# Kernel optimization log

Hardware: AMD Instinct MI355X
Metric: run time of the kernel (lower is better)

Reference implementation:

```python
import jax, jax.numpy as jnp
import numpy as np

N_NODES = 50000
NEG_SLOPE = 0.2  # PyG GATConv leaky_relu default


def _gat_layer(x, src, dst, W, a_src, a_dst, bias, heads, ch):
    n = x.shape[0]
    h = (x @ W).reshape(n, heads, ch)                    # [N,H,C]
    alpha_s = jnp.sum(h * a_src, axis=-1)                # [N,H]
    alpha_d = jnp.sum(h * a_dst, axis=-1)                # [N,H]
    e = alpha_s[src] + alpha_d[dst]                      # [E,H]
    e = jnp.where(e > 0, e, NEG_SLOPE * e)               # leaky_relu
    # segment softmax over incoming edges of each dst node
    m = jax.ops.segment_max(e, dst, num_segments=n)      # [N,H]
    m = jnp.where(jnp.isfinite(m), m, 0.0)
    ex = jnp.exp(e - m[dst])                             # [E,H]
    denom = jax.ops.segment_sum(ex, dst, num_segments=n) # [N,H]
    alpha = ex / (denom[dst] + 1e-16)                    # [E,H]
    msg = alpha[:, :, None] * h[src]                     # [E,H,C]
    out = jax.ops.segment_sum(msg, dst, num_segments=n)  # [N,H,C]
    return out.reshape(n, heads * ch) + bias


def setup_inputs() -> dict:
    key = jax.random.key(0)
    ks = jax.random.split(key, 10)
    F_in, H1, C1, C2 = 256, 8, 32, 32
    E = 500000
    x = jax.random.normal(ks[0], (N_NODES, F_in), dtype=jnp.float32)
    edge_index = jax.random.randint(ks[1], (2, E), 0, N_NODES, dtype=jnp.int64)
    s1 = 1.0 / np.sqrt(F_in)
    s2 = 1.0 / np.sqrt(H1 * C1)
    return {
        "x": x,
        "edge_index": edge_index,
        "W1": jax.random.normal(ks[2], (F_in, H1 * C1), dtype=jnp.float32) * s1,
        "a_src1": jax.random.normal(ks[3], (H1, C1), dtype=jnp.float32) * s2,
        "a_dst1": jax.random.normal(ks[4], (H1, C1), dtype=jnp.float32) * s2,
        "b1": jnp.zeros((H1 * C1,), dtype=jnp.float32),
        "W2": jax.random.normal(ks[5], (H1 * C1, C2), dtype=jnp.float32) * s2,
        "a_src2": jax.random.normal(ks[6], (1, C2), dtype=jnp.float32) * (1.0 / np.sqrt(C2)),
        "a_dst2": jax.random.normal(ks[7], (1, C2), dtype=jnp.float32) * (1.0 / np.sqrt(C2)),
        "b2": jnp.zeros((C2,), dtype=jnp.float32),
    }


def reference(x, edge_index, W1, a_src1, a_dst1, b1, W2, a_src2, a_dst2, b2):
    n = x.shape[0]
    # add self-loops (PyG GATConv default add_self_loops=True)
    loop = jnp.arange(n, dtype=edge_index.dtype)
    src = jnp.concatenate([edge_index[0], loop])
    dst = jnp.concatenate([edge_index[1], loop])
    h = _gat_layer(x, src, dst, W1, a_src1, a_dst1, b1, heads=8, ch=32)
    h = jax.nn.elu(h)
    h = _gat_layer(h, src, dst, W2, a_src2, a_dst2, b2, heads=1, ch=32)
    return jax.nn.log_softmax(h, axis=1)
```

## Files before the change

kernel.cpp:

```cpp
#include <hip/hip_runtime.h>
#include <math.h>


typedef __attribute__((ext_vector_type(8))) short bf16x8;
typedef __attribute__((ext_vector_type(4))) float f32x4;

__device__ __forceinline__ float bf2f(ushort u) {
    union { uint i; float f; } v; v.i = ((uint)u) << 16; return v.f;
}
__device__ __forceinline__ ushort f2bf(float f) {
    union { float f; uint i; } v; v.f = f;
    uint r = v.i + 0x7FFFu + ((v.i >> 16) & 1u);
    return (ushort)(r >> 16);
}
__device__ __forceinline__ uint pack2(float a, float b) {
    return (uint)f2bf(a) | ((uint)f2bf(b) << 16);
}

__global__ void detect_kernel(const int* ei32, int* flag) {
    __shared__ int cnt;
    if (threadIdx.x == 0) cnt = 0;
    __syncthreads();
    int nz = 0;
    for (int i = threadIdx.x; i < 1024; i += blockDim.x)
        if (ei32[2 * i + 1] != 0) nz++;
    atomicAdd(&cnt, nz);
    __syncthreads();
    if (threadIdx.x == 0) *flag = (cnt > 16) ? 1 : 0;
}

__global__ void decode_degree_kernel(const void* ei, int E, int ET, int N,
                                     const int* __restrict__ flag,
                                     int* __restrict__ src, int* __restrict__ dst,
                                     int* __restrict__ deg) {
    int k = blockIdx.x * blockDim.x + threadIdx.x;
    if (k >= ET) return;
    int s, d;
    if (k < E) {
        if (*flag) {
            const int* p = (const int*)ei;
            s = p[k]; d = p[E + k];
        } else {
            const long long* p = (const long long*)ei;
            s = (int)p[k]; d = (int)p[E + k];
        }
    } else {
        s = d = k - E;
    }
    s = min(max(s, 0), N - 1);
    d = min(max(d, 0), N - 1);
    src[k] = s; dst[k] = d;
    atomicAdd(&deg[d], 1);
}

__global__ __launch_bounds__(256) void scanA_kernel(const int* __restrict__ deg,
                                                    int* __restrict__ bsum, int n) {
    int i = blockIdx.x * 256 + threadIdx.x;
    int v = (i < n) ? deg[i] : 0;
#pragma unroll
    for (int s = 1; s < 64; s <<= 1) v += __shfl_xor(v, s, 64);
    __shared__ int ws[4];
    int lane = threadIdx.x & 63, wid = threadIdx.x >> 6;
    if (lane == 0) ws[wid] = v;
    __syncthreads();
    if (threadIdx.x == 0) bsum[blockIdx.x] = ws[0] + ws[1] + ws[2] + ws[3];
}

__global__ __launch_bounds__(1024) void scanB_kernel(int* __restrict__ bsum, int nb) {
    int t = threadIdx.x;
    int v = (t < nb) ? bsum[t] : 0;
    __shared__ int sm[1024];
    sm[t] = v;
    __syncthreads();
    for (int s = 1; s < 1024; s <<= 1) {
        int a = (t >= s) ? sm[t - s] : 0;
        __syncthreads();
        sm[t] += a;
        __syncthreads();
    }
    if (t < nb) bsum[t] = sm[t] - v;
}

__global__ __launch_bounds__(256) void scanC_kernel(const int* __restrict__ deg,
                                                    const int* __restrict__ bsum,
                                                    int* __restrict__ off, int n) {
    int t = threadIdx.x;
    int i = blockIdx.x * 256 + t;
    int v = (i < n) ? deg[i] : 0;
    int incl = v;
    int lane = t & 63, wid = t >> 6;
#pragma unroll
    for (int s = 1; s < 64; s <<= 1) {
        int a = __shfl_up(incl, s, 64);
        if (lane >= s) incl += a;
    }
    __shared__ int wsum[4];
    if (lane == 63) wsum[wid] = incl;
    __syncthreads();
    int wo = 0;
    for (int w = 0; w < wid; w++) wo += wsum[w];
    if (i < n) off[i + 1] = bsum[blockIdx.x] + wo + incl;
    if (i == 0) off[0] = 0;
}

__global__ void scatter_kernel(const int* __restrict__ src, const int* __restrict__ dst,
                               int ET, const int* __restrict__ off,
                               int* __restrict__ cursor, int* __restrict__ esrc) {
    int k = blockIdx.x * blockDim.x + threadIdx.x;
    if (k >= ET) return;
    int d = dst[k];
    int p = atomicAdd(&cursor[d], 1);
    esrc[off[d] + p] = src[k];
}

__global__ __launch_bounds__(256) void convert_w_kernel(
        const float* __restrict__ W1, const float* __restrict__ W2,
        ushort* __restrict__ w1t, ushort* __restrict__ w2t) {
    int bid = blockIdx.x;
    if (bid < 64) {
        __shared__ float tile[32][33];
        int tx = threadIdx.x & 31, ty = threadIdx.x >> 5;
        int bx = bid & 7, by = bid >> 3;
        for (int i = 0; i < 32; i += 8)
            tile[ty + i][tx] = W1[(by * 32 + ty + i) * 256 + bx * 32 + tx];
        __syncthreads();
        for (int i = 0; i < 32; i += 8)
            w1t[(bx * 32 + ty + i) * 256 + by * 32 + tx] = f2bf(tile[tx][ty + i]);
    } else {
        int idx = (bid - 64) * 256 + threadIdx.x;
        int c = idx >> 8, k = idx & 255;
        w2t[idx] = f2bf(W2[k * 32 + c]);
    }
}

#define LDA 72
__global__ __launch_bounds__(256) void gemm1_mfma(
        const float* __restrict__ x,
        const ushort* __restrict__ w1t,
        ushort* __restrict__ h1b,
        int N) {
    __shared__ ushort Al[128 * LDA];
    __shared__ ushort Bl[128 * LDA];
    int t = threadIdx.x;
    int row0 = blockIdx.x * 128;
    int n0 = blockIdx.y * 128;
    int lane = t & 63, wid = t >> 6;
    int wr = wid >> 1, wc = wid & 1;

    f32x4 acc[4][4] = {};

    int sr = t >> 1, scs = (t & 1) * 32;
    for (int k0 = 0; k0 < 256; k0 += 64) {
        {
            int gr = row0 + sr;
            float4 f[8];
            if (gr < N) {
                const float4* g = (const float4*)(x + (size_t)gr * 256 + k0 + scs);
#pragma unroll
                for (int q = 0; q < 8; q++) f[q] = g[q];
            } else {
#pragma unroll
                for (int q = 0; q < 8; q++) f[q] = float4{0.f, 0.f, 0.f, 0.f};
            }
            uint4* d = (uint4*)&Al[sr * LDA + scs];
#pragma unroll
            for (int p = 0; p < 4; p++) {
                uint4 u;
                u.x = pack2(f[2 * p].x, f[2 * p].y);
                u.y = pack2(f[2 * p].z, f[2 * p].w);
                u.z = pack2(f[2 * p + 1].x, f[2 * p + 1].y);
                u.w = pack2(f[2 * p + 1].z, f[2 * p + 1].w);
                d[p] = u;
            }
        }
        {
            const uint4* g = (const uint4*)(w1t + (size_t)(n0 + sr) * 256 + k0 + scs);
            uint4* d = (uint4*)&Bl[sr * LDA + scs];
            d[0] = g[0]; d[1] = g[1]; d[2] = g[2]; d[3] = g[3];
        }
        __syncthreads();

#pragma unroll
        for (int ks = 0; ks < 2; ks++) {
            int kk = ks * 32 + (lane >> 4) * 8;
            bf16x8 af[4], bfr[4];
#pragma unroll
            for (int mi = 0; mi < 4; mi++) {
                int r = wr * 64 + mi * 16 + (lane & 15);
                af[mi] = *(const bf16x8*)&Al[r * LDA + kk];
            }
#pragma unroll
            for (int ni = 0; ni < 4; ni++) {
                int r = wc * 64 + ni * 16 + (lane & 15);
                bfr[ni] = *(const bf16x8*)&Bl[r * LDA + kk];
            }
#pragma unroll
            for (int mi = 0; mi < 4; mi++)
#pragma unroll
                for (int ni = 0; ni < 4; ni++)
                    acc[mi][ni] = __builtin_amdgcn_mfma_f32_16x16x32_bf16(
                        af[mi], bfr[ni], acc[mi][ni], 0, 0, 0);
        }
        __syncthreads();
    }

#pragma unroll
    for (int mi = 0; mi < 4; mi++)
#pragma unroll
        for (int ni = 0; ni < 4; ni++) {
            int gc = n0 + wc * 64 + ni * 16 + (lane & 15);
#pragma unroll
            for (int j = 0; j < 4; j++) {
                int gr = row0 + wr * 64 + mi * 16 + (lane >> 4) * 4 + j;
                if (gr < N) h1b[(size_t)gr * 256 + gc] = f2bf(acc[mi][ni][j]);
            }
        }
}

__global__ __launch_bounds__(256) void alpha1_kernel(
        const ushort* __restrict__ h1b,
        const float* __restrict__ a_src1, const float* __restrict__ a_dst1,
        float* __restrict__ as1, float* __restrict__ ad1, int N) {
    int t = threadIdx.x;
    int g = t >> 5, l = t & 31;
    int node = blockIdx.x * 8 + g;
    if (node >= N) return;
    bf16x8 hv = *(const bf16x8*)&h1b[(size_t)node * 256 + l * 8];
    float s = 0.f, d = 0.f;
#pragma unroll
    for (int i = 0; i < 8; i++) {
        float h = bf2f((ushort)hv[i]);
        s = fmaf(h, a_src1[l * 8 + i], s);
        d = fmaf(h, a_dst1[l * 8 + i], d);
    }
    s += __shfl_xor(s, 1); s += __shfl_xor(s, 2);
    d += __shfl_xor(d, 1); d += __shfl_xor(d, 2);
    if ((l & 3) == 0) {
        as1[node * 8 + (l >> 2)] = s;
        ad1[node * 8 + (l >> 2)] = d;
    }
}

#define FMA8(W, V)                                                      \
    c0 = fmaf(W, bf2f((ushort)((V).x & 0xffffu)), c0);                  \
    c1 = fmaf(W, bf2f((ushort)((V).x >> 16)), c1);                      \
    c2 = fmaf(W, bf2f((ushort)((V).y & 0xffffu)), c2);                  \
    c3 = fmaf(W, bf2f((ushort)((V).y >> 16)), c3);                      \
    c4 = fmaf(W, bf2f((ushort)((V).z & 0xffffu)), c4);                  \
    c5 = fmaf(W, bf2f((ushort)((V).z >> 16)), c5);                      \
    c6 = fmaf(W, bf2f((ushort)((V).w & 0xffffu)), c6);                  \
    c7 = fmaf(W, bf2f((ushort)((V).w >> 16)), c7);

__global__ __launch_bounds__(256) void agg1f_kernel(
        const ushort* __restrict__ h1b,
        const float* __restrict__ as1, const float* __restrict__ ad1,
        const float* __restrict__ b1,
        const int* __restrict__ off, const int* __restrict__ esrc,
        ushort* __restrict__ hactb, int N) {
    __shared__ float s_w[8][32][8];
    int t = threadIdx.x;
    int slot = t >> 5;
    int node = blockIdx.x * 8 + slot;
    int l = t & 31;
    if (node >= N) return;
    int beg = off[node], end = off[node + 1];
    int deg = end - beg;
    int h = l & 7, q = l >> 3;
    float adv = ad1[node * 8 + h];
    int head2 = l >> 2;
    int ch0 = l * 8;
    const ushort* hb = h1b + ch0;
    float c0 = 0.f, c1 = 0.f, c2 = 0.f, c3 = 0.f;
    float c4 = 0.f, c5 = 0.f, c6 = 0.f, c7 = 0.f;

    if (deg <= 32) {
        float e_r[8];
#pragma unroll
        for (int r = 0; r < 8; r++) {
            int j = beg + r * 4 + q;
            float e = -3.0e38f;
            if (j < end) {
                e = as1[esrc[j] * 8 + h] + adv;
                e = (e > 0.f) ? e : 0.2f * e;
            }
            e_r[r] = e;
        }
        float m = e_r[0];
#pragma unroll
        for (int r = 1; r < 8; r++) m = fmaxf(m, e_r[r]);
        m = fmaxf(m, __shfl_xor(m, 8, 32));
        m = fmaxf(m, __shfl_xor(m, 16, 32));
        float dnm = 0.f;
#pragma unroll
        for (int r = 0; r < 8; r++)
            if (beg + r * 4 + q < end) dnm += __expf(e_r[r] - m);
        dnm += __shfl_xor(dnm, 8, 32);
        dnm += __shfl_xor(dnm, 16, 32);
        float inv = 1.f / (dnm + 1e-16f);
#pragma unroll
        for (int r = 0; r < 8; r++) {
            int j = beg + r * 4 + q;
            if (j < end) s_w[slot][r * 4 + q][h] = __expf(e_r[r] - m) * inv;
        }
        const float* wp = &s_w[slot][0][head2];
        int j = beg;
        for (; j + 4 <= end; j += 4) {
            int k = j - beg;
            int s0 = esrc[j + 0], s1 = esrc[j + 1], s2 = esrc[j + 2], s3 = esrc[j + 3];
            float w0 = wp[(k + 0) * 8];
            float w1 = wp[(k + 1) * 8];
            float w2 = wp[(k + 2) * 8];
            float w3 = wp[(k + 3) * 8];
            uint4 v0 = *(const uint4*)(hb + (size_t)s0 * 256);
            uint4 v1 = *(const uint4*)(hb + (size_t)s1 * 256);
            uint4 v2 = *(const uint4*)(hb + (size_t)s2 * 256);
            uint4 v3 = *(const uint4*)(hb + (size_t)s3 * 256);
            FMA8(w0, v0);
            FMA8(w1, v1);
            FMA8(w2, v2);
            FMA8(w3, v3);
        }
        for (; j < end; j++) {
            int s0 = esrc[j];
            float w = wp[(j - beg) * 8];
            uint4 v = *(const uint4*)(hb + (size_t)s0 * 256);
            FMA8(w, v);
        }
    } else {
        float m = -3.0e38f;
        for (int j0 = beg; j0 < end; j0 += 4) {
            int j = j0 + q;
            if (j < end) {
                float e = as1[esrc[j] * 8 + h] + adv;
                e = (e > 0.f) ? e : 0.2f * e;
                m = fmaxf(m, e);
            }
        }
        m = fmaxf(m, __shfl_xor(m, 8, 32));
        m = fmaxf(m, __shfl_xor(m, 16, 32));
        float dnm = 0.f;
        for (int j0 = beg; j0 < end; j0 += 4) {
            int j = j0 + q;
            if (j < end) {
                float e = as1[esrc[j] * 8 + h] + adv;
                e = (e > 0.f) ? e : 0.2f * e;
                dnm += __expf(e - m);
            }
        }
        dnm += __shfl_xor(dnm, 8, 32);
        dnm += __shfl_xor(dnm, 16, 32);
        float inv = 1.f / (dnm + 1e-16f);
        float m2   = __shfl(m, head2, 32);
        float inv2 = __shfl(inv, head2, 32);
        float adv2 = __shfl(adv, head2, 32);
        const float* asp = as1 + head2;
        for (int j = beg; j < end; j++) {
            int s0 = esrc[j];
            float e = asp[s0 * 8] + adv2;
            e = (e > 0.f) ? e : 0.2f * e;
            float w = __expf(e - m2) * inv2;
            uint4 v = *(const uint4*)(hb + (size_t)s0 * 256);
            FMA8(w, v);
        }
    }

    float4 bv0 = *(const float4*)&b1[ch0];
    float4 bv1 = *(const float4*)&b1[ch0 + 4];
    float o0 = c0 + bv0.x, o1 = c1 + bv0.y, o2 = c2 + bv0.z, o3 = c3 + bv0.w;
    float o4 = c4 + bv1.x, o5 = c5 + bv1.y, o6 = c6 + bv1.z, o7 = c7 + bv1.w;
    o0 = (o0 > 0.f) ? o0 : (__expf(o0) - 1.f);
    o1 = (o1 > 0.f) ? o1 : (__expf(o1) - 1.f);
    o2 = (o2 > 0.f) ? o2 : (__expf(o2) - 1.f);
    o3 = (o3 > 0.f) ? o3 : (__expf(o3) - 1.f);
    o4 = (o4 > 0.f) ? o4 : (__expf(o4) - 1.f);
    o5 = (o5 > 0.f) ? o5 : (__expf(o5) - 1.f);
    o6 = (o6 > 0.f) ? o6 : (__expf(o6) - 1.f);
    o7 = (o7 > 0.f) ? o7 : (__expf(o7) - 1.f);
    uint4 r;
    r.x = pack2(o0, o1);
    r.y = pack2(o2, o3);
    r.z = pack2(o4, o5);
    r.w = pack2(o6, o7);
    *(uint4*)(hactb + (size_t)node * 256 + ch0) = r;
}

__global__ __launch_bounds__(256) void gemm2_mfma(
        const ushort* __restrict__ hactb,
        const ushort* __restrict__ w2t,
        float* __restrict__ h2, int N) {
    __shared__ ushort Al[128 * LDA];
    __shared__ ushort Bl[32 * LDA];
    int t = threadIdx.x;
    int row0 = blockIdx.x * 128;
    int lane = t & 63, wid = t >> 6;

    f32x4 acc[2][2] = {};

    int sr = t >> 1, scs = (t & 1) * 32;
    for (int k0 = 0; k0 < 256; k0 += 64) {
        {
            int gr = row0 + sr;
            uint4 v0 = {0,0,0,0}, v1 = {0,0,0,0}, v2 = {0,0,0,0}, v3 = {0,0,0,0};
            if (gr < N) {
                const uint4* g = (const uint4*)(hactb + (size_t)gr * 256 + k0 + scs);
                v0 = g[0]; v1 = g[1]; v2 = g[2]; v3 = g[3];
            }
            uint4* d = (uint4*)&Al[sr * LDA + scs];
            d[0] = v0; d[1] = v1; d[2] = v2; d[3] = v3;
        }
        if (t < 64) {
            const uint4* g = (const uint4*)(w2t + (size_t)sr * 256 + k0 + scs);
            uint4* d = (uint4*)&Bl[sr * LDA + scs];
            d[0] = g[0]; d[1] = g[1]; d[2] = g[2]; d[3] = g[3];
        }
        __syncthreads();

#pragma unroll
        for (int ks = 0; ks < 2; ks++) {
            int kk = ks * 32 + (lane >> 4) * 8;
            bf16x8 af[2], bfr[2];
#pragma unroll
            for (int mi = 0; mi < 2; mi++) {
                int r = wid * 32 + mi * 16 + (lane & 15);
                af[mi] = *(const bf16x8*)&Al[r * LDA + kk];
            }
#pragma unroll
            for (int ni = 0; ni < 2; ni++) {
                int r = ni * 16 + (lane & 15);
                bfr[ni] = *(const bf16x8*)&Bl[r * LDA + kk];
            }
#pragma unroll
            for (int mi = 0; mi < 2; mi++)
#pragma unroll
                for (int ni = 0; ni < 2; ni++)
                    acc[mi][ni] = __builtin_amdgcn_mfma_f32_16x16x32_bf16(
                        af[mi], bfr[ni], acc[mi][ni], 0, 0, 0);
        }
        __syncthreads();
    }

#pragma unroll
    for (int mi = 0; mi < 2; mi++)
#pragma unroll
        for (int ni = 0; ni < 2; ni++) {
            int gc = ni * 16 + (lane & 15);
#pragma unroll
            for (int j = 0; j < 4; j++) {
                int gr = row0 + wid * 32 + mi * 16 + (lane >> 4) * 4 + j;
                if (gr < N) h2[(size_t)gr * 32 + gc] = acc[mi][ni][j];
            }
        }
}

__global__ __launch_bounds__(256) void alpha2_kernel(
        const float* __restrict__ h2,
        const float* __restrict__ a_src2, const float* __restrict__ a_dst2,
        float* __restrict__ as2, float* __restrict__ ad2, int N) {
    int t = threadIdx.x;
    int g = t >> 3, q = t & 7;
    int node = blockIdx.x * 32 + g;
    if (node >= N) return;
    float4 v = *(const float4*)&h2[(size_t)node * 32 + q * 4];
    float4 sa = *(const float4*)&a_src2[q * 4];
    float4 da = *(const float4*)&a_dst2[q * 4];
    float s = v.x * sa.x + v.y * sa.y + v.z * sa.z + v.w * sa.w;
    float d = v.x * da.x + v.y * da.y + v.z * da.z + v.w * da.w;
    s += __shfl_xor(s, 1, 8); s += __shfl_xor(s, 2, 8); s += __shfl_xor(s, 4, 8);
    d += __shfl_xor(d, 1, 8); d += __shfl_xor(d, 2, 8); d += __shfl_xor(d, 4, 8);
    if (q == 0) { as2[node] = s; ad2[node] = d; }
}

__global__ __launch_bounds__(256) void agg2f_kernel(
        const float* __restrict__ h2,
        const float* __restrict__ as2, const float* __restrict__ ad2,
        const float* __restrict__ b2,
        const int* __restrict__ off, const int* __restrict__ esrc,
        float* __restrict__ out, int N) {
    __shared__ float s_w[8][32];
    int t = threadIdx.x;
    int g = t >> 5, c = t & 31;
    int node = blockIdx.x * 8 + g;
    if (node >= N) return;
    int beg = off[node], end = off[node + 1];
    int deg = end - beg;
    float adv = ad2[node];
    const float* hcol = h2 + c;
    float a0 = 0.f, a1 = 0.f, a2 = 0.f, a3 = 0.f;

    if (deg <= 32) {
        float e = -3.0e38f;
        if (c < deg) {
            float v = as2[esrc[beg + c]] + adv;
            e = (v > 0.f) ? v : 0.2f * v;
        }
        float m = e;
#pragma unroll
        for (int s = 16; s > 0; s >>= 1) m = fmaxf(m, __shfl_xor(m, s, 32));
        float w = (c < deg) ? __expf(e - m) : 0.f;
        float dn = w;
#pragma unroll
        for (int s = 16; s > 0; s >>= 1) dn += __shfl_xor(dn, s, 32);
        s_w[g][c] = w * (1.f / (dn + 1e-16f));
        int j = beg;
        for (; j + 4 <= end; j += 4) {
            int k = j - beg;
            int s0 = esrc[j + 0], s1 = esrc[j + 1], s2 = esrc[j + 2], s3 = esrc[j + 3];
            float w0 = s_w[g][k + 0];
            float w1 = s_w[g][k + 1];
            float w2 = s_w[g][k + 2];
            float w3 = s_w[g][k + 3];
            a0 = fmaf(w0, hcol[(size_t)s0 * 32], a0);
            a1 = fmaf(w1, hcol[(size_t)s1 * 32], a1);
            a2 = fmaf(w2, hcol[(size_t)s2 * 32], a2);
            a3 = fmaf(w3, hcol[(size_t)s3 * 32], a3);
        }
        for (; j < end; j++)
            a0 = fmaf(s_w[g][j - beg], hcol[(size_t)esrc[j] * 32], a0);
    } else {
        float m = -3.0e38f, dnm = 0.f;
        for (int base = beg; base < end; base += 32) {
            int n_ch = min(32, end - base);
            float ej = -3.0e38f;
            if (c < n_ch) {
                float e = as2[esrc[base + c]] + adv;
                ej = (e > 0.f) ? e : 0.2f * e;
            }
            float cm = ej;
#pragma unroll
            for (int s = 16; s > 0; s >>= 1) cm = fmaxf(cm, __shfl_xor(cm, s, 32));
            float nm = fmaxf(m, cm);
            float scl = __expf(m - nm);
            float wj = (c < n_ch) ? __expf(ej - nm) : 0.f;
            float ws = wj;
#pragma unroll
            for (int s = 16; s > 0; s >>= 1) ws += __shfl_xor(ws, s, 32);
            dnm = dnm * scl + ws;
            m = nm;
        }
        float inv = 1.f / (dnm + 1e-16f);
        int j = beg;
        for (; j + 4 <= end; j += 4) {
            int s0 = esrc[j + 0], s1 = esrc[j + 1], s2 = esrc[j + 2], s3 = esrc[j + 3];
            float e0 = as2[s0] + adv, e1 = as2[s1] + adv;
            float e2 = as2[s2] + adv, e3 = as2[s3] + adv;
            e0 = (e0 > 0.f) ? e0 : 0.2f * e0;
            e1 = (e1 > 0.f) ? e1 : 0.2f * e1;
            e2 = (e2 > 0.f) ? e2 : 0.2f * e2;
            e3 = (e3 > 0.f) ? e3 : 0.2f * e3;
            float w0 = __expf(e0 - m) * inv, w1 = __expf(e1 - m) * inv;
            float w2 = __expf(e2 - m) * inv, w3 = __expf(e3 - m) * inv;
            a0 = fmaf(w0, hcol[(size_t)s0 * 32], a0);
            a1 = fmaf(w1, hcol[(size_t)s1 * 32], a1);
            a2 = fmaf(w2, hcol[(size_t)s2 * 32], a2);
            a3 = fmaf(w3, hcol[(size_t)s3 * 32], a3);
        }
        for (; j < end; j++) {
            int s0 = esrc[j];
            float e = as2[s0] + adv;
            e = (e > 0.f) ? e : 0.2f * e;
            a0 = fmaf(__expf(e - m) * inv, hcol[(size_t)s0 * 32], a0);
        }
    }

    float v = (a0 + a1) + (a2 + a3) + b2[c];
    float mx = v;
#pragma unroll
    for (int s = 16; s > 0; s >>= 1) mx = fmaxf(mx, __shfl_xor(mx, s, 32));
    float sum = __expf(v - mx);
#pragma unroll
    for (int s = 16; s > 0; s >>= 1) sum += __shfl_xor(sum, s, 32);
    out[(size_t)node * 32 + c] = (v - mx) - __logf(sum);
}

extern "C" void kernel_launch(void* const* d_in, const int* in_sizes, int n_in,
                              void* d_out, int out_size, void* d_ws, size_t ws_size,
                              hipStream_t stream) {
    const float* x      = (const float*)d_in[0];
    const void*  ei     = d_in[1];
    const float* W1     = (const float*)d_in[2];
    const float* a_src1 = (const float*)d_in[3];
    const float* a_dst1 = (const float*)d_in[4];
    const float* b1     = (const float*)d_in[5];
    const float* W2     = (const float*)d_in[6];
    const float* a_src2 = (const float*)d_in[7];
    const float* a_dst2 = (const float*)d_in[8];
    const float* b2     = (const float*)d_in[9];
    const int N  = in_sizes[0] / 256;
    const int E  = in_sizes[1] / 2;
    const int ET = E + N;
    float* outp = (float*)d_out;
    (void)n_in; (void)out_size; (void)ws_size;

    char* ws = (char*)d_ws;
    size_t o = 0;
    auto alloc = [&](size_t bytes) -> void* {
        void* p = ws + o;
        o += (bytes + 255) & ~(size_t)255;
        return p;
    };
    int*    flag   = (int*)alloc(4);
    int*    src32  = (int*)alloc((size_t)ET * 4);
    int*    dst32  = (int*)alloc((size_t)ET * 4);
    int*    deg    = (int*)alloc((size_t)2 * N * 4);
    int*    cursor = deg + N;
    int*    off    = (int*)alloc((size_t)(N + 1) * 4);
    int*    esrc   = (int*)alloc((size_t)ET * 4);
    int*    bsum   = (int*)alloc((size_t)1024 * 4);
    ushort* w1t    = (ushort*)alloc((size_t)256 * 256 * 2);
    ushort* w2t    = (ushort*)alloc((size_t)32 * 256 * 2);
    ushort* h1b    = (ushort*)alloc((size_t)N * 256 * 2);
    float*  as1    = (float*)alloc((size_t)N * 8 * 4);
    float*  ad1    = (float*)alloc((size_t)N * 8 * 4);
    ushort* hactb  = (ushort*)alloc((size_t)N * 256 * 2);
    float*  h2     = (float*)alloc((size_t)N * 32 * 4);
    float*  as2    = (float*)alloc((size_t)N * 4);
    float*  ad2    = (float*)alloc((size_t)N * 4);

    const int nbScan = (N + 255) / 256;

    hipMemsetAsync(deg, 0, (size_t)2 * N * 4, stream);
    detect_kernel<<<1, 256, 0, stream>>>((const int*)ei, flag);
    decode_degree_kernel<<<(ET + 255) / 256, 256, 0, stream>>>(ei, E, ET, N, flag,
                                                               src32, dst32, deg);
    scanA_kernel<<<nbScan, 256, 0, stream>>>(deg, bsum, N);
    scanB_kernel<<<1, 1024, 0, stream>>>(bsum, nbScan);
    scanC_kernel<<<nbScan, 256, 0, stream>>>(deg, bsum, off, N);
    scatter_kernel<<<(ET + 255) / 256, 256, 0, stream>>>(src32, dst32, ET, off,
                                                         cursor, esrc);

    convert_w_kernel<<<96, 256, 0, stream>>>(W1, W2, w1t, w2t);

    gemm1_mfma<<<dim3((N + 127) / 128, 2), 256, 0, stream>>>(x, w1t, h1b, N);
    alpha1_kernel<<<(N + 7) / 8, 256, 0, stream>>>(h1b, a_src1, a_dst1, as1, ad1, N);
    agg1f_kernel<<<(N + 7) / 8, 256, 0, stream>>>(h1b, as1, ad1, b1, off, esrc,
                                                  hactb, N);
    gemm2_mfma<<<(N + 127) / 128, 256, 0, stream>>>(hactb, w2t, h2, N);
    alpha2_kernel<<<(N + 31) / 32, 256, 0, stream>>>(h2, a_src2, a_dst2, as2, ad2, N);
    agg2f_kernel<<<(N + 7) / 8, 256, 0, stream>>>(h2, as2, ad2, b2, off, esrc,
                                                  outp, N);
}
```

Baseline: 196.3 us.

## Fuse attention-score dot products into GEMM epilogues and widen gemm1 tile

The alpha1 and alpha2 kernels are removed. Their per-head dot products with a_src/a_dst are now computed in the epilogues of gemm1 and gemm2 from fp32 accumulators, reduced with wave shuffles. gemm1 now covers all 256 output columns per block instead of two column blocks, so x is read and converted once. The cost is double the LDS for B and twice the accumulator registers, which may lower occupancy, and the scores now come from fp32 rather than bf16-rounded values.

```diff
diff --git a/kernel.cpp b/kernel.cpp
--- a/kernel.cpp
+++ b/kernel.cpp
@@ -137,17 +137,18 @@
 __global__ __launch_bounds__(256) void gemm1_mfma(
         const float* __restrict__ x,
         const ushort* __restrict__ w1t,
+        const float* __restrict__ a_src1, const float* __restrict__ a_dst1,
         ushort* __restrict__ h1b,
+        float* __restrict__ as1, float* __restrict__ ad1,
         int N) {
     __shared__ ushort Al[128 * LDA];
-    __shared__ ushort Bl[128 * LDA];
+    __shared__ ushort Bl[256 * LDA];
     int t = threadIdx.x;
     int row0 = blockIdx.x * 128;
-    int n0 = blockIdx.y * 128;
     int lane = t & 63, wid = t >> 6;
     int wr = wid >> 1, wc = wid & 1;
 
-    f32x4 acc[4][4] = {};
+    f32x4 acc[4][8] = {};
 
     int sr = t >> 1, scs = (t & 1) * 32;
     for (int k0 = 0; k0 < 256; k0 += 64) {
@@ -174,71 +175,76 @@
             }
         }
         {
-            const uint4* g = (const uint4*)(w1t + (size_t)(n0 + sr) * 256 + k0 + scs);
-            uint4* d = (uint4*)&Bl[sr * LDA + scs];
-            d[0] = g[0]; d[1] = g[1]; d[2] = g[2]; d[3] = g[3];
+            const uint4* g = (const uint4*)(w1t + (size_t)t * 256 + k0);
+            uint4* d = (uint4*)&Bl[t * LDA];
+#pragma unroll
+            for (int p = 0; p < 8; p++) d[p] = g[p];
         }
         __syncthreads();
 
 #pragma unroll
         for (int ks = 0; ks < 2; ks++) {
             int kk = ks * 32 + (lane >> 4) * 8;
-            bf16x8 af[4], bfr[4];
+            bf16x8 af[4];
 #pragma unroll
             for (int mi = 0; mi < 4; mi++) {
                 int r = wr * 64 + mi * 16 + (lane & 15);
                 af[mi] = *(const bf16x8*)&Al[r * LDA + kk];
             }
 #pragma unroll
-            for (int ni = 0; ni < 4; ni++) {
-                int r = wc * 64 + ni * 16 + (lane & 15);
-                bfr[ni] = *(const bf16x8*)&Bl[r * LDA + kk];
-            }
-#pragma unroll
-            for (int mi = 0; mi < 4; mi++)
-#pragma unroll
-                for (int ni = 0; ni < 4; ni++)
+            for (int ni = 0; ni < 8; ni++) {
+                int br = wc * 128 + ni * 16 + (lane & 15);
+                bf16x8 bfr = *(const bf16x8*)&Bl[br * LDA + kk];
+#pragma unroll
+                for (int mi = 0; mi < 4; mi++)
                     acc[mi][ni] = __builtin_amdgcn_mfma_f32_16x16x32_bf16(
-                        af[mi], bfr[ni], acc[mi][ni], 0, 0, 0);
+                        af[mi], bfr, acc[mi][ni], 0, 0, 0);
+            }
         }
         __syncthreads();
     }
 
+    int l16 = lane & 15, l4 = lane >> 4;
 #pragma unroll
     for (int mi = 0; mi < 4; mi++)
 #pragma unroll
-        for (int ni = 0; ni < 4; ni++) {
-            int gc = n0 + wc * 64 + ni * 16 + (lane & 15);
+        for (int ni = 0; ni < 8; ni++) {
+            int gc = wc * 128 + ni * 16 + l16;
 #pragma unroll
             for (int j = 0; j < 4; j++) {
-                int gr = row0 + wr * 64 + mi * 16 + (lane >> 4) * 4 + j;
+                int gr = row0 + wr * 64 + mi * 16 + l4 * 4 + j;
                 if (gr < N) h1b[(size_t)gr * 256 + gc] = f2bf(acc[mi][ni][j]);
             }
         }
-}
-
-__global__ __launch_bounds__(256) void alpha1_kernel(
-        const ushort* __restrict__ h1b,
-        const float* __restrict__ a_src1, const float* __restrict__ a_dst1,
-        float* __restrict__ as1, float* __restrict__ ad1, int N) {
-    int t = threadIdx.x;
-    int g = t >> 5, l = t & 31;
-    int node = blockIdx.x * 8 + g;
-    if (node >= N) return;
-    bf16x8 hv = *(const bf16x8*)&h1b[(size_t)node * 256 + l * 8];
-    float s = 0.f, d = 0.f;
-#pragma unroll
-    for (int i = 0; i < 8; i++) {
-        float h = bf2f((ushort)hv[i]);
-        s = fmaf(h, a_src1[l * 8 + i], s);
-        d = fmaf(h, a_dst1[l * 8 + i], d);
-    }
-    s += __shfl_xor(s, 1); s += __shfl_xor(s, 2);
-    d += __shfl_xor(d, 1); d += __shfl_xor(d, 2);
-    if ((l & 3) == 0) {
-        as1[node * 8 + (l >> 2)] = s;
-        ad1[node * 8 + (l >> 2)] = d;
-    }
+
+    float sa[8], da[8];
+#pragma unroll
+    for (int ni = 0; ni < 8; ni++) {
+        int c = wc * 128 + ni * 16 + l16;
+        sa[ni] = a_src1[c];
+        da[ni] = a_dst1[c];
+    }
+#pragma unroll
+    for (int mi = 0; mi < 4; mi++)
+#pragma unroll
+        for (int j = 0; j < 4; j++) {
+            int gr = row0 + wr * 64 + mi * 16 + l4 * 4 + j;
+#pragma unroll
+            for (int h = 0; h < 4; h++) {
+                float ps = acc[mi][2 * h][j] * sa[2 * h]
+                         + acc[mi][2 * h + 1][j] * sa[2 * h + 1];
+                float pd = acc[mi][2 * h][j] * da[2 * h]
+                         + acc[mi][2 * h + 1][j] * da[2 * h + 1];
+                ps += __shfl_xor(ps, 1); ps += __shfl_xor(ps, 2);
+                ps += __shfl_xor(ps, 4); ps += __shfl_xor(ps, 8);
+                pd += __shfl_xor(pd, 1); pd += __shfl_xor(pd, 2);
+                pd += __shfl_xor(pd, 4); pd += __shfl_xor(pd, 8);
+                if (l16 == 0 && gr < N) {
+                    as1[gr * 8 + wc * 4 + h] = ps;
+                    ad1[gr * 8 + wc * 4 + h] = pd;
+                }
+            }
+        }
 }
 
 #define FMA8(W, V)                                                      \
@@ -387,7 +393,9 @@
 __global__ __launch_bounds__(256) void gemm2_mfma(
         const ushort* __restrict__ hactb,
         const ushort* __restrict__ w2t,
-        float* __restrict__ h2, int N) {
+        const float* __restrict__ a_src2, const float* __restrict__ a_dst2,
+        float* __restrict__ h2,
+        float* __restrict__ as2, float* __restrict__ ad2, int N) {
     __shared__ ushort Al[128 * LDA];
     __shared__ ushort Bl[32 * LDA];
     int t = threadIdx.x;
@@ -439,35 +447,37 @@
         __syncthreads();
     }
 
+    int l16 = lane & 15, l4 = lane >> 4;
 #pragma unroll
     for (int mi = 0; mi < 2; mi++)
 #pragma unroll
         for (int ni = 0; ni < 2; ni++) {
-            int gc = ni * 16 + (lane & 15);
+            int gc = ni * 16 + l16;
 #pragma unroll
             for (int j = 0; j < 4; j++) {
-                int gr = row0 + wid * 32 + mi * 16 + (lane >> 4) * 4 + j;
+                int gr = row0 + wid * 32 + mi * 16 + l4 * 4 + j;
                 if (gr < N) h2[(size_t)gr * 32 + gc] = acc[mi][ni][j];
             }
         }
-}
-
-__global__ __launch_bounds__(256) void alpha2_kernel(
-        const float* __restrict__ h2,
-        const float* __restrict__ a_src2, const float* __restrict__ a_dst2,
-        float* __restrict__ as2, float* __restrict__ ad2, int N) {
-    int t = threadIdx.x;
-    int g = t >> 3, q = t & 7;
-    int node = blockIdx.x * 32 + g;
-    if (node >= N) return;
-    float4 v = *(const float4*)&h2[(size_t)node * 32 + q * 4];
-    float4 sa = *(const float4*)&a_src2[q * 4];
-    float4 da = *(const float4*)&a_dst2[q * 4];
-    float s = v.x * sa.x + v.y * sa.y + v.z * sa.z + v.w * sa.w;
-    float d = v.x * da.x + v.y * da.y + v.z * da.z + v.w * da.w;
-    s += __shfl_xor(s, 1, 8); s += __shfl_xor(s, 2, 8); s += __shfl_xor(s, 4, 8);
-    d += __shfl_xor(d, 1, 8); d += __shfl_xor(d, 2, 8); d += __shfl_xor(d, 4, 8);
-    if (q == 0) { as2[node] = s; ad2[node] = d; }
+
+    float sa0 = a_src2[l16], sa1 = a_src2[16 + l16];
+    float da0 = a_dst2[l16], da1 = a_dst2[16 + l16];
+#pragma unroll
+    for (int mi = 0; mi < 2; mi++)
+#pragma unroll
+        for (int j = 0; j < 4; j++) {
+            int gr = row0 + wid * 32 + mi * 16 + l4 * 4 + j;
+            float ps = acc[mi][0][j] * sa0 + acc[mi][1][j] * sa1;
+            float pd = acc[mi][0][j] * da0 + acc[mi][1][j] * da1;
+            ps += __shfl_xor(ps, 1); ps += __shfl_xor(ps, 2);
+            ps += __shfl_xor(ps, 4); ps += __shfl_xor(ps, 8);
+            pd += __shfl_xor(pd, 1); pd += __shfl_xor(pd, 2);
+            pd += __shfl_xor(pd, 4); pd += __shfl_xor(pd, 8);
+            if (l16 == 0 && gr < N) {
+                as2[gr] = ps;
+                ad2[gr] = pd;
+            }
+        }
 }
 
 __global__ __launch_bounds__(256) void agg2f_kernel(
@@ -630,12 +640,12 @@
 
     convert_w_kernel<<<96, 256, 0, stream>>>(W1, W2, w1t, w2t);
 
-    gemm1_mfma<<<dim3((N + 127) / 128, 2), 256, 0, stream>>>(x, w1t, h1b, N);
-    alpha1_kernel<<<(N + 7) / 8, 256, 0, stream>>>(h1b, a_src1, a_dst1, as1, ad1, N);
+    gemm1_mfma<<<(N + 127) / 128, 256, 0, stream>>>(x, w1t, a_src1, a_dst1,
+                                                    h1b, as1, ad1, N);
     agg1f_kernel<<<(N + 7) / 8, 256, 0, stream>>>(h1b, as1, ad1, b1, off, esrc,
                                                   hactb, N);
-    gemm2_mfma<<<(N + 127) / 128, 256, 0, stream>>>(hactb, w2t, h2, N);
-    alpha2_kernel<<<(N + 31) / 32, 256, 0, stream>>>(h2, a_src2, a_dst2, as2, ad2, N);
+    gemm2_mfma<<<(N + 127) / 128, 256, 0, stream>>>(hactb, w2t, a_src2, a_dst2,
+                                                    h2, as2, ad2, N);
     agg2f_kernel<<<(N + 7) / 8, 256, 0, stream>>>(h2, as2, ad2, b2, off, esrc,
                                                   outp, N);
 }
```

Measured after the change: 213.6 us. 1.09x slower.
